# Kernel optimization log

Hardware: AMD Instinct MI355X
Metric: run time of the kernel (lower is better)

Reference implementation:

```python
import jax, jax.numpy as jnp
import numpy as np
import math

MODEL_DIM = 1024
BATCH = 4
SEQ = 4096
ATTENTION_INPUT = 'both'


def make_F(model_dim, attention_input):
    F = jnp.zeros((model_dim, model_dim), dtype=jnp.float32)
    if attention_input == 'both':
        a = model_dim
    else:
        a = model_dim // 2
    # faithful to source: elif means 'both' only hits the first branch
    if attention_input in ['both', 'only_sem']:
        idx = jnp.arange(0, a)
        F = F.at[idx, idx].set(1.0)
    elif attention_input in ['only_pos']:
        idx = jnp.arange(a, 2 * a)
        F = F.at[idx, idx].set(1.0)
    return F


def setup_inputs() -> dict:
    key = jax.random.key(0)
    kx, kq, kk, kv = jax.random.split(key, 4)
    x = jax.random.normal(kx, (BATCH, SEQ, MODEL_DIM), dtype=jnp.float32)
    Q = jax.random.normal(kq, (MODEL_DIM, MODEL_DIM), dtype=jnp.float32) / math.sqrt(MODEL_DIM)
    K = jax.random.normal(kk, (MODEL_DIM, MODEL_DIM), dtype=jnp.float32) / math.sqrt(MODEL_DIM)
    V = jax.random.normal(kv, (MODEL_DIM, MODEL_DIM), dtype=jnp.float32) / math.sqrt(MODEL_DIM)
    return {"x": x, "Q": Q, "K": K, "V": V}


def reference(x, Q, K, V):
    model_dim = Q.shape[0]
    F = make_F(model_dim, ATTENTION_INPUT)
    Qx = x @ F @ Q            # [B, S, D]
    Kx = x @ F @ K            # [B, S, D]
    Vx = x @ V                # [B, S, D]
    scores = jnp.einsum('bqd,bkd->bqk', Qx, Kx) / math.sqrt(model_dim)  # [B, S, S]
    seq = x.shape[1]
    causal_mask = jnp.triu(jnp.ones((seq, seq), dtype=bool), k=1)       # True above diagonal
    scores = jnp.where(causal_mask, -jnp.inf, scores)
    probs = jax.nn.softmax(scores, axis=-1)
    return jnp.einsum('bqk,bkd->bqd', probs, Vx)
```

## Files before the change

kernel.cpp:

```cpp
#include <hip/hip_runtime.h>
#include <cstdint>
#include <cstddef>
#include <cmath>


typedef unsigned short u16;
typedef __bf16  bf16x8 __attribute__((ext_vector_type(8)));
typedef float   f32x4  __attribute__((ext_vector_type(4)));
typedef unsigned short u16x4 __attribute__((ext_vector_type(4)));

typedef __attribute__((address_space(1))) void gvoid;
typedef __attribute__((address_space(3))) void lvoid;

__device__ __forceinline__ u16 f2bf(float f) {
  union { float f; unsigned u; } v; v.f = f;
  unsigned u = v.u;
  u += 0x7FFFu + ((u >> 16) & 1u);
  return (u16)(u >> 16);
}
__device__ __forceinline__ float bf2f(u16 h) {
  union { unsigned u; float f; } v; v.u = ((unsigned)h) << 16;
  return v.f;
}
__device__ __forceinline__ void async16(const void* g, void* l) {
  __builtin_amdgcn_global_load_lds((gvoid*)(void*)g, (lvoid*)l, 16, 0, 0);
}

__global__ void __launch_bounds__(256) cvt_f32_bf16(const float4* __restrict__ in,
                                                    u16* __restrict__ out, int n4) {
  int i = blockIdx.x * 256 + threadIdx.x;
  if (i >= n4) return;
  float4 v = in[i];
  u16x4 o = { f2bf(v.x), f2bf(v.y), f2bf(v.z), f2bf(v.w) };
  *(u16x4*)(out + 4 * (size_t)i) = o;
}

__device__ __forceinline__ u16 to_bfs(float v, float s) { return f2bf(v * s); }
__device__ __forceinline__ u16 to_bfs(u16 v, float)     { return v; }

template <typename TIN>
__global__ void __launch_bounds__(256) transpose_to_bf16(
    const TIN* __restrict__ in, u16* __restrict__ out,
    int rows, int cols, long inStride, long outStride, float scale) {
  __shared__ u16 t[64][68];
  int rt = blockIdx.x * 64, ct = blockIdx.y * 64;
  long ib = (long)blockIdx.z * inStride, ob = (long)blockIdx.z * outStride;
  int tx = threadIdx.x & 63, ty = threadIdx.x >> 6;
#pragma unroll
  for (int r = ty; r < 64; r += 4)
    t[r][tx] = to_bfs(in[ib + (long)(rt + r) * cols + ct + tx], scale);
  __syncthreads();
#pragma unroll
  for (int r = ty; r < 64; r += 4)
    out[ob + (long)(ct + r) * rows + rt + tx] = t[tx][r];
}

template <bool OUTF32, bool TRI, bool CK>
__global__ void __launch_bounds__(256, 2) gemm_bt(
    const u16* __restrict__ A, const u16* __restrict__ Bt, void* __restrict__ C,
    int K, int lda, int ldb, int ldc,
    long aStride, long bStride, long cStride, float alpha) {
  int mt, nt;
  if (TRI) {
    const int bid = blockIdx.x;
    int m = (int)((sqrtf(4.0f * (float)bid + 1.0f) - 1.0f) * 0.5f);
    while ((m + 1) * (m + 2) <= bid) ++m;
    while (m * (m + 1) > bid) --m;
    mt = m; nt = bid - m * (m + 1);
  } else {
    mt = CK ? (int)(gridDim.x - 1 - blockIdx.x) : (int)blockIdx.x;
    nt = blockIdx.y;
  }
  const int bz = blockIdx.z;
  const int tid = threadIdx.x, wv = tid >> 6, ln = tid & 63;
  const u16* Ag = A + (long)bz * aStride + (long)(mt * 256) * lda;
  const u16* Bg = Bt + (long)bz * bStride + (long)(nt * 128) * ldb;

  __shared__ __align__(16) __bf16 As[2][256 * 32];
  __shared__ __align__(16) __bf16 Bs[2][128 * 32];

  f32x4 acc[8][4];
#pragma unroll
  for (int i = 0; i < 8; ++i)
#pragma unroll
    for (int j = 0; j < 4; ++j)
#pragma unroll
      for (int r = 0; r < 4; ++r) acc[i][j][r] = 0.f;

  const int kend = CK ? (((mt + 1) * 256 < K) ? (mt + 1) * 256 : K) : K;
  const int wm = wv & 1, wn = wv >> 1;
  const int mrow = wm * 128, nrow = wn * 64;
  const int lr = ln & 15, quad = ln >> 4;

  long aOff[4]; int aLds[4];
#pragma unroll
  for (int q = 0; q < 4; ++q) {
    int c = q * 256 + tid, row = c >> 2, c8i = c & 3;
    aOff[q] = (long)row * lda + ((c8i ^ ((row >> 1) & 3)) << 3);
    aLds[q] = c * 8;
  }
  long bOff[2]; int bLds[2];
#pragma unroll
  for (int q = 0; q < 2; ++q) {
    int c = q * 256 + tid, row = c >> 2, c8i = c & 3;
    bOff[q] = (long)row * ldb + ((c8i ^ ((row >> 1) & 3)) << 3);
    bLds[q] = c * 8;
  }
  const int swq = (quad ^ ((lr >> 1) & 3)) << 3;

  for (int k0 = 0; k0 < kend; k0 += 64) {
#pragma unroll
    for (int p = 0; p < 2; ++p) {
      const long kk = k0 + p * 32;
#pragma unroll
      for (int q = 0; q < 4; ++q)
        async16(Ag + kk + aOff[q], (char*)As[p] + aLds[q] * 2);
#pragma unroll
      for (int q = 0; q < 2; ++q)
        async16(Bg + kk + bOff[q], (char*)Bs[p] + bLds[q] * 2);
    }
    __syncthreads();
#pragma unroll
    for (int p = 0; p < 2; ++p) {
      bf16x8 af[8], bfr[4];
#pragma unroll
      for (int u = 0; u < 8; ++u)
        af[u] = *(const bf16x8*)&As[p][(mrow + u * 16 + lr) * 32 + swq];
#pragma unroll
      for (int j = 0; j < 4; ++j)
        bfr[j] = *(const bf16x8*)&Bs[p][(nrow + j * 16 + lr) * 32 + swq];
#pragma unroll
      for (int u = 0; u < 8; ++u)
#pragma unroll
        for (int j = 0; j < 4; ++j)
          acc[u][j] = __builtin_amdgcn_mfma_f32_16x16x32_bf16(af[u], bfr[j], acc[u][j], 0, 0, 0);
    }
    __syncthreads();
  }

  const long cb = (long)bz * cStride;
#pragma unroll
  for (int i = 0; i < 8; ++i) {
    int row0 = mt * 256 + mrow + i * 16 + quad * 4;
#pragma unroll
    for (int j = 0; j < 4; ++j) {
      int col = nt * 128 + nrow + j * 16 + lr;
#pragma unroll
      for (int r = 0; r < 4; ++r) {
        float v = acc[i][j][r] * alpha;
        long idx = cb + (long)(row0 + r) * ldc + col;
        if (OUTF32) ((float*)C)[idx] = v;
        else        ((u16*)C)[idx]  = f2bf(v);
      }
    }
  }
}

__global__ void __launch_bounds__(256) softmax_rows(u16* __restrict__ Sb,
                                                    long bStride, int S) {
  const int row = blockIdx.x;
  u16* p = Sb + (long)blockIdx.y * bStride + (long)row * S;
  const int L = row + 1;
  const int Lpad = (L + 255) & ~255;
  const int tid = threadIdx.x, ln = tid & 63, wv = tid >> 6;
  __shared__ float red[8];

  float vals[16];
  float lmax = -3.4e38f;
#pragma unroll
  for (int k = 0; k < 16; ++k) {
    int j = tid + k * 256;
    if (j < L) { float v = bf2f(p[j]); vals[k] = v; lmax = fmaxf(lmax, v); }
  }
#pragma unroll
  for (int o = 32; o > 0; o >>= 1) lmax = fmaxf(lmax, __shfl_down(lmax, o));
  if (ln == 0) red[wv] = lmax;
  __syncthreads();
  float m = fmaxf(fmaxf(red[0], red[1]), fmaxf(red[2], red[3]));

  float lsum = 0.f;
#pragma unroll
  for (int k = 0; k < 16; ++k) {
    int j = tid + k * 256;
    if (j < L) { float e = __expf(vals[k] - m); vals[k] = e; lsum += e; }
  }
#pragma unroll
  for (int o = 32; o > 0; o >>= 1) lsum += __shfl_down(lsum, o);
  __syncthreads();
  if (ln == 0) red[wv] = lsum;
  __syncthreads();
  float inv = 1.f / (red[0] + red[1] + red[2] + red[3]);
#pragma unroll
  for (int k = 0; k < 16; ++k) {
    int j = tid + k * 256;
    if (j < L) p[j] = f2bf(vals[k] * inv);
  }
  for (int j = L + tid; j < Lpad; j += 256) p[j] = 0;
}

extern "C" void kernel_launch(void* const* d_in, const int* in_sizes, int n_in,
                              void* d_out, int out_size, void* d_ws, size_t ws_size,
                              hipStream_t stream) {
  const float* x = (const float*)d_in[0];
  const float* Q = (const float*)d_in[1];
  const float* K = (const float*)d_in[2];
  const float* V = (const float*)d_in[3];
  float* out = (float*)d_out;

  constexpr int  Bb = 4, S = 4096, D = 1024;
  constexpr long MB = 1024 * 1024;
  if (ws_size < (size_t)(224 * MB)) return;

  char* ws = (char*)d_ws;
  u16* QKx  = (u16*)(ws);
  u16* Vxt  = (u16*)(ws + 64 * MB);
  u16* Sb   = (u16*)(ws + 96 * MB);
  u16* Vtmp = (u16*)(ws + 96 * MB);
  u16* XB   = (u16*)(ws + 128 * MB);
  u16* WTqk = (u16*)(ws + 160 * MB);
  u16* WTv  = (u16*)(ws + 164 * MB);

  const long SD = (long)S * D, SS = (long)S * S;

  cvt_f32_bf16<<<dim3((Bb * S * D / 4) / 256), 256, 0, stream>>>(
      (const float4*)x, XB, Bb * S * D / 4);

  transpose_to_bf16<float><<<dim3(16, 16, 1), 256, 0, stream>>>(
      Q, WTqk, 1024, 1024, 0, 0, 0.03125f);
  transpose_to_bf16<float><<<dim3(16, 16, 1), 256, 0, stream>>>(
      K, WTqk + 1024 * 1024, 1024, 1024, 0, 0, 1.0f);
  transpose_to_bf16<float><<<dim3(16, 16, 1), 256, 0, stream>>>(
      V, WTv, 1024, 1024, 0, 0, 1.0f);

  gemm_bt<false, false, false><<<dim3(64, 16, 1), 256, 0, stream>>>(
      XB, WTqk, QKx, 1024, 1024, 1024, 2048, 0, 0, 0, 1.0f);
  gemm_bt<false, false, false><<<dim3(64, 8, 1), 256, 0, stream>>>(
      XB, WTv, Vtmp, 1024, 1024, 1024, 1024, 0, 0, 0, 1.0f);

  transpose_to_bf16<u16><<<dim3(64, 16, Bb), 256, 0, stream>>>(
      Vtmp, Vxt, S, D, SD, SD, 1.0f);

  gemm_bt<false, true, false><<<dim3(272, 1, Bb), 256, 0, stream>>>(
      QKx, QKx + 1024, Sb, 1024, 2048, 2048, S, 2 * SD, 2 * SD, SS, 1.0f);

  softmax_rows<<<dim3(S, Bb), 256, 0, stream>>>(Sb, SS, S);

  gemm_bt<true, false, true><<<dim3(16, 8, Bb), 256, 0, stream>>>(
      Sb, Vxt, out, S, S, S, D, SS, SD, SD, 1.0f);
}
```

Before: 526.4 us.

## Shrink PV GEMM tile to 128 rows and balance causal work across blocks

Makes the GEMM M-tile a template parameter and runs the final probs×V GEMM with 128-row tiles, launching 1024 blocks instead of 512. A custom block-id mapping interleaves long and short causal rows so heavy and light tiles are spread across the dispatch order. Smaller tiles allow higher occupancy (launch bound of 4) and less tail imbalance, in exchange for lower data reuse per block and more B-tile reloads.

```diff
diff --git a/kernel.cpp b/kernel.cpp
--- a/kernel.cpp
+++ b/kernel.cpp
@@ -55,46 +55,52 @@
     out[ob + (long)(ct + r) * rows + rt + tx] = t[tx][r];
 }
 
-template <bool OUTF32, bool TRI, bool CK>
-__global__ void __launch_bounds__(256, 2) gemm_bt(
+template <bool OUTF32, bool TRI, bool CK, int BM>
+__global__ void __launch_bounds__(256, BM == 256 ? 2 : 4) gemm_bt(
     const u16* __restrict__ A, const u16* __restrict__ Bt, void* __restrict__ C,
     int K, int lda, int ldb, int ldc,
     long aStride, long bStride, long cStride, float alpha) {
-  int mt, nt;
+  constexpr int MR = BM / 32;
+  constexpr int AQ = BM / 64;
+  int mt, nt, bz;
   if (TRI) {
     const int bid = blockIdx.x;
     int m = (int)((sqrtf(4.0f * (float)bid + 1.0f) - 1.0f) * 0.5f);
     while ((m + 1) * (m + 2) <= bid) ++m;
     while (m * (m + 1) > bid) --m;
     mt = m; nt = bid - m * (m + 1);
+    bz = blockIdx.z;
+  } else if (CK) {
+    const int id = blockIdx.x;
+    const int g = id & 7, mid = (id >> 3) & 31, hi = id >> 8;
+    bz = mid & 3; nt = mid >> 2;
+    mt = (hi == 0) ? 31 - g : (hi == 1) ? 16 + g : (hi == 2) ? 15 - g : g;
   } else {
-    mt = CK ? (int)(gridDim.x - 1 - blockIdx.x) : (int)blockIdx.x;
-    nt = blockIdx.y;
-  }
-  const int bz = blockIdx.z;
+    mt = blockIdx.x; nt = blockIdx.y; bz = blockIdx.z;
+  }
   const int tid = threadIdx.x, wv = tid >> 6, ln = tid & 63;
-  const u16* Ag = A + (long)bz * aStride + (long)(mt * 256) * lda;
+  const u16* Ag = A + (long)bz * aStride + (long)(mt * BM) * lda;
   const u16* Bg = Bt + (long)bz * bStride + (long)(nt * 128) * ldb;
 
-  __shared__ __align__(16) __bf16 As[2][256 * 32];
+  __shared__ __align__(16) __bf16 As[2][BM * 32];
   __shared__ __align__(16) __bf16 Bs[2][128 * 32];
 
-  f32x4 acc[8][4];
-#pragma unroll
-  for (int i = 0; i < 8; ++i)
+  f32x4 acc[MR][4];
+#pragma unroll
+  for (int i = 0; i < MR; ++i)
 #pragma unroll
     for (int j = 0; j < 4; ++j)
 #pragma unroll
       for (int r = 0; r < 4; ++r) acc[i][j][r] = 0.f;
 
-  const int kend = CK ? (((mt + 1) * 256 < K) ? (mt + 1) * 256 : K) : K;
+  const int kend = CK ? (((mt + 1) * BM < K) ? (mt + 1) * BM : K) : K;
   const int wm = wv & 1, wn = wv >> 1;
-  const int mrow = wm * 128, nrow = wn * 64;
+  const int mrow = wm * (BM / 2), nrow = wn * 64;
   const int lr = ln & 15, quad = ln >> 4;
 
-  long aOff[4]; int aLds[4];
-#pragma unroll
-  for (int q = 0; q < 4; ++q) {
+  long aOff[AQ]; int aLds[AQ];
+#pragma unroll
+  for (int q = 0; q < AQ; ++q) {
     int c = q * 256 + tid, row = c >> 2, c8i = c & 3;
     aOff[q] = (long)row * lda + ((c8i ^ ((row >> 1) & 3)) << 3);
     aLds[q] = c * 8;
@@ -113,7 +119,7 @@
     for (int p = 0; p < 2; ++p) {
       const long kk = k0 + p * 32;
 #pragma unroll
-      for (int q = 0; q < 4; ++q)
+      for (int q = 0; q < AQ; ++q)
         async16(Ag + kk + aOff[q], (char*)As[p] + aLds[q] * 2);
 #pragma unroll
       for (int q = 0; q < 2; ++q)
@@ -122,15 +128,15 @@
     __syncthreads();
 #pragma unroll
     for (int p = 0; p < 2; ++p) {
-      bf16x8 af[8], bfr[4];
-#pragma unroll
-      for (int u = 0; u < 8; ++u)
+      bf16x8 af[MR], bfr[4];
+#pragma unroll
+      for (int u = 0; u < MR; ++u)
         af[u] = *(const bf16x8*)&As[p][(mrow + u * 16 + lr) * 32 + swq];
 #pragma unroll
       for (int j = 0; j < 4; ++j)
         bfr[j] = *(const bf16x8*)&Bs[p][(nrow + j * 16 + lr) * 32 + swq];
 #pragma unroll
-      for (int u = 0; u < 8; ++u)
+      for (int u = 0; u < MR; ++u)
 #pragma unroll
         for (int j = 0; j < 4; ++j)
           acc[u][j] = __builtin_amdgcn_mfma_f32_16x16x32_bf16(af[u], bfr[j], acc[u][j], 0, 0, 0);
@@ -140,8 +146,8 @@
 
   const long cb = (long)bz * cStride;
 #pragma unroll
-  for (int i = 0; i < 8; ++i) {
-    int row0 = mt * 256 + mrow + i * 16 + quad * 4;
+  for (int i = 0; i < MR; ++i) {
+    int row0 = mt * BM + mrow + i * 16 + quad * 4;
 #pragma unroll
     for (int j = 0; j < 4; ++j) {
       int col = nt * 128 + nrow + j * 16 + lr;
@@ -232,19 +238,19 @@
   transpose_to_bf16<float><<<dim3(16, 16, 1), 256, 0, stream>>>(
       V, WTv, 1024, 1024, 0, 0, 1.0f);
 
-  gemm_bt<false, false, false><<<dim3(64, 16, 1), 256, 0, stream>>>(
+  gemm_bt<false, false, false, 256><<<dim3(64, 16, 1), 256, 0, stream>>>(
       XB, WTqk, QKx, 1024, 1024, 1024, 2048, 0, 0, 0, 1.0f);
-  gemm_bt<false, false, false><<<dim3(64, 8, 1), 256, 0, stream>>>(
+  gemm_bt<false, false, false, 256><<<dim3(64, 8, 1), 256, 0, stream>>>(
       XB, WTv, Vtmp, 1024, 1024, 1024, 1024, 0, 0, 0, 1.0f);
 
   transpose_to_bf16<u16><<<dim3(64, 16, Bb), 256, 0, stream>>>(
       Vtmp, Vxt, S, D, SD, SD, 1.0f);
 
-  gemm_bt<false, true, false><<<dim3(272, 1, Bb), 256, 0, stream>>>(
+  gemm_bt<false, true, false, 256><<<dim3(272, 1, Bb), 256, 0, stream>>>(
       QKx, QKx + 1024, Sb, 1024, 2048, 2048, S, 2 * SD, 2 * SD, SS, 1.0f);
 
   softmax_rows<<<dim3(S, Bb), 256, 0, stream>>>(Sb, SS, S);
 
-  gemm_bt<true, false, true><<<dim3(16, 8, Bb), 256, 0, stream>>>(
+  gemm_bt<true, false, true, 128><<<dim3(1024, 1, 1), 256, 0, stream>>>(
       Sb, Vxt, out, S, S, S, D, SS, SD, SD, 1.0f);
 }
```

After: 504.9 us. 4.1% less time.
